# Kernel tuning notes

Measured on AMD Instinct MI355X. Metric: run time of the kernel, lower is better.

The kernel has to match this reference:

```python
import jax, jax.numpy as jnp
import numpy as np

# Compressed weight shape [O, I] represents a dense [m=2*O, k=2*I] matrix:
#  - 1:2 structured row sparsity: `indices` [O] gives the nonzero dense row ids
#  - 2:4 structured col sparsity: `metadata` [O, I] gives, for each compressed
#    element, its position (0..3) within its group of 4 dense columns
O, I = 4096, 2048          # compressed weight dims (out_features, in_features)
M_DIM, K_DIM = 2 * O, 2 * I  # dense GEMM dims m, k
N_TOK = 4096               # n = input.shape[0]
K_ACT = 2048               # number of active activation rows (multiple of 64)
PAD_MULT = 64


def setup_inputs() -> dict:
    key = jax.random.key(0)
    k1, k2, k3, k4, k5 = jax.random.split(key, 5)
    inp = jax.random.normal(k1, (N_TOK, K_ACT), dtype=jnp.float32)
    # unique, sorted active-feature indices into the dense k dimension
    idx = jnp.sort(jax.random.permutation(k2, K_DIM)[:K_ACT]).astype(jnp.int32)
    # compressed N:M weight values (original uses torch.rand -> uniform [0,1))
    weight = jax.random.uniform(k3, (O, I), dtype=jnp.float32)
    # 1:2 row sparsity: which O of the m dense rows are nonzero
    indices = jnp.sort(jax.random.permutation(k4, M_DIM)[:O]).astype(jnp.int32)
    # 2:4 metadata: per group of 4 dense columns, 2 distinct sorted positions
    G = I // 2
    scores = jax.random.uniform(k5, (O, G, 4))
    metadata = jnp.sort(jnp.argsort(scores, axis=-1)[..., :2], axis=-1)
    metadata = metadata.reshape(O, I).astype(jnp.int32)
    return {"input": inp, "idx": idx, "weight": weight,
            "indices": indices, "metadata": metadata}


def _padding_idx(idx, mult):
    # pad index list to a multiple of `mult` (static shapes)
    pad = (-idx.shape[0]) % mult
    return jnp.pad(idx, (0, pad)), pad


def reference(input, idx, weight, indices, metadata):
    O_, I_ = weight.shape
    m, k, n = 2 * O_, 2 * I_, input.shape[0]
    # ---- decompress N:M weight to dense [m, k] ----
    group_base = (jnp.arange(I_) // 2) * 4                 # [I]
    dense_cols = group_base[None, :] + metadata            # [O, I] in [0, k)
    W = jnp.zeros((m, k), weight.dtype).at[indices[:, None], dense_cols].set(weight)
    # ---- decompress sparse activation to dense B [k, n] ----
    idx_p, pad = _padding_idx(idx, PAD_MULT)
    vals = jnp.pad(input, ((0, 0), (0, pad)))              # [n, K_act+pad]
    B = jnp.zeros((k, n), input.dtype).at[idx_p].add(vals.T)
    # ---- sparse-sparse GEMM (dense-equivalent reference) ----
    return W @ B                                           # [m, n]
```

## Files before the change

### kernel.cpp

```cpp
#include <hip/hip_runtime.h>
#include <hip/hip_bf16.h>
#include <stdint.h>

#define O_DIM   4096
#define I_DIM   2048
#define M_DENSE 8192
#define K_DENSE 4096
#define N_TOK   4096
#define K_ACT   2048

typedef __bf16 bf16x8 __attribute__((ext_vector_type(8)));
typedef float  f32x4  __attribute__((ext_vector_type(4)));

__device__ __forceinline__ unsigned f2bf(float f) {
    unsigned u = __builtin_bit_cast(unsigned, f);
    return (u + 0x7FFFu + ((u >> 16) & 1u)) >> 16;
}

__device__ __forceinline__ void load16(const unsigned short* g, unsigned short* l) {
    __builtin_amdgcn_global_load_lds(
        (__attribute__((address_space(1))) void*)(g),
        (__attribute__((address_space(3))) void*)(l),
        16, 0, 0);
}

__global__ __launch_bounds__(256) void prep(const float* __restrict__ weight,
                                            const int* __restrict__ metadata,
                                            const int* __restrict__ idx,
                                            const float* __restrict__ input,
                                            uint4* __restrict__ A2,
                                            uint4* __restrict__ Bbt) {
    if (blockIdx.x >= O_DIM) {
        int gid = (blockIdx.x - O_DIM) * 256 + threadIdx.x;
        const float4* in = (const float4*)input;
        float4 a = in[2 * gid], b = in[2 * gid + 1];
        uint4 u;
        u.x = f2bf(a.x) | (f2bf(a.y) << 16);
        u.y = f2bf(a.z) | (f2bf(a.w) << 16);
        u.z = f2bf(b.x) | (f2bf(b.y) << 16);
        u.w = f2bf(b.z) | (f2bf(b.w) << 16);
        Bbt[gid] = u;
        return;
    }
    __shared__ int   smeta[I_DIM];
    __shared__ float sw[I_DIM];
    int o = blockIdx.x;
    const int4*   mrow = (const int4*)(metadata + (size_t)o * I_DIM);
    const float4* wrow = (const float4*)(weight + (size_t)o * I_DIM);
#pragma unroll
    for (int it = 0; it < I_DIM / 4 / 256; ++it) {
        int i = it * 256 + threadIdx.x;
        *(int4*)(smeta + i * 4) = mrow[i];
        *(float4*)(sw + i * 4)  = wrow[i];
    }
    __syncthreads();
    int j0 = threadIdx.x * 8;
    int4 c0 = *(const int4*)(idx + j0);
    int4 c1 = *(const int4*)(idx + j0 + 4);
    int cs[8] = {c0.x, c0.y, c0.z, c0.w, c1.x, c1.y, c1.z, c1.w};
    unsigned r[8];
#pragma unroll
    for (int u = 0; u < 8; ++u) {
        int c = cs[u];
        int g2 = (c >> 2) * 2;
        int pos = c & 3;
        int m0v = smeta[g2], m1v = smeta[g2 + 1];
        float v = (m0v == pos) ? sw[g2] : ((m1v == pos) ? sw[g2 + 1] : 0.0f);
        r[u] = f2bf(v);
    }
    uint4 packed;
    packed.x = r[0] | (r[1] << 16);
    packed.y = r[2] | (r[3] << 16);
    packed.z = r[4] | (r[5] << 16);
    packed.w = r[6] | (r[7] << 16);
    A2[((size_t)o * K_ACT + j0) >> 3] = packed;
}

__global__ __launch_bounds__(256, 4) void gemm_scatter(
        const unsigned short* __restrict__ A,
        const unsigned short* __restrict__ Bt,
        const int* __restrict__ indices,
        float* __restrict__ out) {
    constexpr int N = N_TOK, K = K_ACT;
    constexpr int TM = 128, TN = 128, BK = 32;
    __shared__ alignas(16) unsigned short sA[TM * BK];
    __shared__ alignas(16) unsigned short sB[TN * BK];
    __shared__ int s_list[256];
    __shared__ int s_cnt;

    const int t    = threadIdx.x;
    const int wave = t >> 6;
    const int lane = t & 63;
    const int m0 = blockIdx.y * TM;
    const int n0 = blockIdx.x * TN;

    {
        if (t == 0) s_cnt = 0;
        int r = blockIdx.y * 256 + t;
        int lo = 0, hi = O_DIM;
        while (lo < hi) { int mid = (lo + hi) >> 1; if (indices[mid] < r) lo = mid + 1; else hi = mid; }
        bool inactive = !(lo < O_DIM && indices[lo] == r);
        __syncthreads();
        if (inactive) { int p = atomicAdd(&s_cnt, 1); s_list[p] = r; }
        __syncthreads();
        int nin = s_cnt;
        float4 z4 = {0.f, 0.f, 0.f, 0.f};
        for (int task = t; task < nin * 32; task += 256) {
            int row = s_list[task >> 5];
            int c4  = task & 31;
            *(float4*)(out + (size_t)row * N + n0 + c4 * 4) = z4;
        }
    }

    const int fa0 = t, fa1 = t + 256;
    const unsigned short* gA0 = A  + (size_t)(m0 + (fa0 >> 2)) * K + (fa0 & 3) * 8;
    const unsigned short* gA1 = A  + (size_t)(m0 + (fa1 >> 2)) * K + (fa1 & 3) * 8;
    const unsigned short* gB0 = Bt + (size_t)(n0 + (fa0 >> 2)) * K + (fa0 & 3) * 8;
    const unsigned short* gB1 = Bt + (size_t)(n0 + (fa1 >> 2)) * K + (fa1 & 3) * 8;

    unsigned short* lA0 = sA + wave * 512;
    unsigned short* lA1 = sA + 2048 + wave * 512;
    unsigned short* lB0 = sB + wave * 512;
    unsigned short* lB1 = sB + 2048 + wave * 512;

    const int wm   = (wave >> 1) * 64;
    const int wn   = (wave & 1) * 64;
    const int quad = lane >> 4;
    const int lr   = lane & 15;
    const int kq   = quad * 8;

    f32x4 acc[4][4] = {};

    for (int kk = 0; kk < K; kk += BK) {
        __syncthreads();
        load16(gA0 + kk, lA0);
        load16(gA1 + kk, lA1);
        load16(gB0 + kk, lB0);
        load16(gB1 + kk, lB1);
        __syncthreads();

        bf16x8 af[4], bf[4];
#pragma unroll
        for (int mi = 0; mi < 4; ++mi)
            af[mi] = *(const bf16x8*)(sA + (wm + mi * 16 + lr) * BK + kq);
#pragma unroll
        for (int ni = 0; ni < 4; ++ni)
            bf[ni] = *(const bf16x8*)(sB + (wn + ni * 16 + lr) * BK + kq);
#pragma unroll
        for (int mi = 0; mi < 4; ++mi)
#pragma unroll
            for (int ni = 0; ni < 4; ++ni)
                acc[mi][ni] = __builtin_amdgcn_mfma_f32_16x16x32_bf16(
                    af[mi], bf[ni], acc[mi][ni], 0, 0, 0);
    }

#pragma unroll
    for (int mi = 0; mi < 4; ++mi) {
#pragma unroll
        for (int r = 0; r < 4; ++r) {
            int gm = m0 + wm + mi * 16 + quad * 4 + r;
            int orow = indices[gm];
            float* op = out + (size_t)orow * N + n0 + wn + lr;
#pragma unroll
            for (int ni = 0; ni < 4; ++ni)
                op[ni * 16] = acc[mi][ni][r];
        }
    }
}

extern "C" void kernel_launch(void* const* d_in, const int* in_sizes, int n_in,
                              void* d_out, int out_size, void* d_ws, size_t ws_size,
                              hipStream_t stream) {
    const float* input    = (const float*)d_in[0];
    const int*   idx      = (const int*)d_in[1];
    const float* weight   = (const float*)d_in[2];
    const int*   indices  = (const int*)d_in[3];
    const int*   metadata = (const int*)d_in[4];
    float* out = (float*)d_out;

    unsigned short* A2  = (unsigned short*)d_ws;
    unsigned short* Bbt = (unsigned short*)((char*)d_ws + (size_t)(16 << 20));

    prep<<<O_DIM + (N_TOK * K_ACT / 8) / 256, 256, 0, stream>>>(
        weight, metadata, idx, input, (uint4*)A2, (uint4*)Bbt);

    dim3 grid(N_TOK / 128, O_DIM / 128);
    gemm_scatter<<<grid, 256, 0, stream>>>(A2, Bbt, indices, out);
}
```

Baseline: 291.2 us.

## Double K tile to 64 and XOR-swizzle LDS layout to avoid bank conflicts

Raises the GEMM K-step from 32 to 64, which halves the number of barrier-separated load/compute iterations and issues twice as many MFMAs per tile. The global-to-LDS load addresses and the fragment reads now use an XOR swizzle on the 16-byte chunk index keyed by row, so the wider 128-byte LDS rows do not cause bank conflicts. LDS use per block doubles, which may reduce occupancy, and there is still no double buffering.

```diff
diff --git a/kernel.cpp b/kernel.cpp
--- a/kernel.cpp
+++ b/kernel.cpp
@@ -82,7 +82,7 @@
         const int* __restrict__ indices,
         float* __restrict__ out) {
     constexpr int N = N_TOK, K = K_ACT;
-    constexpr int TM = 128, TN = 128, BK = 32;
+    constexpr int TM = 128, TN = 128, BK = 64;
     __shared__ alignas(16) unsigned short sA[TM * BK];
     __shared__ alignas(16) unsigned short sB[TN * BK];
     __shared__ int s_list[256];
@@ -112,40 +112,60 @@
         }
     }
 
-    const int fa0 = t, fa1 = t + 256;
-    const unsigned short* gA0 = A  + (size_t)(m0 + (fa0 >> 2)) * K + (fa0 & 3) * 8;
-    const unsigned short* gA1 = A  + (size_t)(m0 + (fa1 >> 2)) * K + (fa1 & 3) * 8;
-    const unsigned short* gB0 = Bt + (size_t)(n0 + (fa0 >> 2)) * K + (fa0 & 3) * 8;
-    const unsigned short* gB1 = Bt + (size_t)(n0 + (fa1 >> 2)) * K + (fa1 & 3) * 8;
-
-    unsigned short* lA0 = sA + wave * 512;
-    unsigned short* lA1 = sA + 2048 + wave * 512;
-    unsigned short* lB0 = sB + wave * 512;
-    unsigned short* lB1 = sB + 2048 + wave * 512;
+    const unsigned short* gA[4];
+    const unsigned short* gB[4];
+#pragma unroll
+    for (int q = 0; q < 4; ++q) {
+        int f = q * 256 + t;
+        int r = f >> 3, s = (f & 7) ^ (r & 7);
+        gA[q] = A  + (size_t)(m0 + r) * K + s * 8;
+        gB[q] = Bt + (size_t)(n0 + r) * K + s * 8;
+    }
+    unsigned short* lA[4];
+    unsigned short* lB[4];
+#pragma unroll
+    for (int q = 0; q < 4; ++q) {
+        lA[q] = sA + q * 2048 + wave * 512;
+        lB[q] = sB + q * 2048 + wave * 512;
+    }
 
     const int wm   = (wave >> 1) * 64;
     const int wn   = (wave & 1) * 64;
     const int quad = lane >> 4;
     const int lr   = lane & 15;
-    const int kq   = quad * 8;
+    const int lr7  = lr & 7;
+    const int k0 = (quad ^ lr7) * 8;
+    const int k1 = k0 ^ 32;
 
     f32x4 acc[4][4] = {};
 
     for (int kk = 0; kk < K; kk += BK) {
         __syncthreads();
-        load16(gA0 + kk, lA0);
-        load16(gA1 + kk, lA1);
-        load16(gB0 + kk, lB0);
-        load16(gB1 + kk, lB1);
+#pragma unroll
+        for (int q = 0; q < 4; ++q) load16(gA[q] + kk, lA[q]);
+#pragma unroll
+        for (int q = 0; q < 4; ++q) load16(gB[q] + kk, lB[q]);
         __syncthreads();
 
         bf16x8 af[4], bf[4];
 #pragma unroll
         for (int mi = 0; mi < 4; ++mi)
-            af[mi] = *(const bf16x8*)(sA + (wm + mi * 16 + lr) * BK + kq);
+            af[mi] = *(const bf16x8*)(sA + (wm + mi * 16 + lr) * BK + k0);
 #pragma unroll
         for (int ni = 0; ni < 4; ++ni)
-            bf[ni] = *(const bf16x8*)(sB + (wn + ni * 16 + lr) * BK + kq);
+            bf[ni] = *(const bf16x8*)(sB + (wn + ni * 16 + lr) * BK + k0);
+#pragma unroll
+        for (int mi = 0; mi < 4; ++mi)
+#pragma unroll
+            for (int ni = 0; ni < 4; ++ni)
+                acc[mi][ni] = __builtin_amdgcn_mfma_f32_16x16x32_bf16(
+                    af[mi], bf[ni], acc[mi][ni], 0, 0, 0);
+#pragma unroll
+        for (int mi = 0; mi < 4; ++mi)
+            af[mi] = *(const bf16x8*)(sA + (wm + mi * 16 + lr) * BK + k1);
+#pragma unroll
+        for (int ni = 0; ni < 4; ++ni)
+            bf[ni] = *(const bf16x8*)(sB + (wn + ni * 16 + lr) * BK + k1);
 #pragma unroll
         for (int mi = 0; mi < 4; ++mi)
 #pragma unroll
```

Result: slower. 307.1 us (+5.5%).
